# Performance work log

Hardware: AMD Instinct MI355X
Metric: run time of the kernel (lower is better)

Reference implementation:

```python
import jax, jax.numpy as jnp
import numpy as np

SHAPES = [(64, 64), (32, 32), (16, 16), (8, 8)]  # (H,W) per level, strides 8..64 of a 512px image
D, NH, NLV, NP, NLAYERS, DFF = 256, 8, 4, 4, 6, 1024
HD = D // NH
B = 4


def setup_inputs() -> dict:
    key = jax.random.key(0)
    ks = jax.random.split(key, 32)
    inp = {}
    for l, (h, w) in enumerate(SHAPES):
        inp[f"src{l}"] = jax.random.normal(ks[l], (B, D, h, w), jnp.float32)
        inp[f"pos{l}"] = jax.random.normal(ks[4 + l], (B, D, h, w), jnp.float32)
    s = 0.02
    p = lambda k, shape: jax.random.normal(k, shape, jnp.float32) * s
    inp["level_embed"] = p(ks[8], (NLV, D))
    inp["W_so"] = p(ks[9], (NLAYERS, D, NH * NLV * NP * 2)); inp["b_so"] = p(ks[10], (NLAYERS, NH * NLV * NP * 2))
    inp["W_aw"] = p(ks[11], (NLAYERS, D, NH * NLV * NP)); inp["b_aw"] = p(ks[12], (NLAYERS, NH * NLV * NP))
    inp["W_v"] = p(ks[13], (NLAYERS, D, D)); inp["b_v"] = p(ks[14], (NLAYERS, D))
    inp["W_o"] = p(ks[15], (NLAYERS, D, D)); inp["b_o"] = p(ks[16], (NLAYERS, D))
    inp["g1"] = jnp.ones((NLAYERS, D)); inp["be1"] = jnp.zeros((NLAYERS, D))
    inp["W_f1"] = p(ks[17], (NLAYERS, D, DFF)); inp["b_f1"] = p(ks[18], (NLAYERS, DFF))
    inp["W_f2"] = p(ks[19], (NLAYERS, DFF, D)); inp["b_f2"] = p(ks[20], (NLAYERS, D))
    inp["g2"] = jnp.ones((NLAYERS, D)); inp["be2"] = jnp.zeros((NLAYERS, D))
    return inp


def _layernorm(x, g, b):
    m = x.mean(-1, keepdims=True)
    v = x.var(-1, keepdims=True)
    return (x - m) * jax.lax.rsqrt(v + 1e-5) * g + b


def _reference_points():
    refs = []
    for (H_, W_) in SHAPES:
        ry = (jnp.arange(H_, dtype=jnp.float32) + 0.5) / H_
        rx = (jnp.arange(W_, dtype=jnp.float32) + 0.5) / W_
        gy, gx = jnp.meshgrid(ry, rx, indexing="ij")
        refs.append(jnp.stack([gx.ravel(), gy.ravel()], -1))
    return jnp.concatenate(refs, 0)  # [S,2] (x,y); valid_ratios==1 so same per level


def _ms_deform_sample(value, loc, aw):
    # value [B,S,NH,HD]; loc [B,S,NH,NLV,NP,2] (x,y in [0,1]); aw [B,S,NH,NLV,NP]
    Bq, S = value.shape[:2]
    v = value.transpose(0, 2, 1, 3)  # [B,NH,S,HD]
    out = jnp.zeros((Bq, NH, S, HD), value.dtype)
    start = 0
    for l, (H_, W_) in enumerate(SHAPES):
        n = H_ * W_
        vl = v[:, :, start:start + n, :]  # [B,NH,H_*W_,HD]
        start += n
        # grid_sample(align_corners=False) semantics: pixel = loc*size - 0.5, zero padding
        x = loc[:, :, :, l, :, 0] * W_ - 0.5  # [B,S,NH,NP]
        y = loc[:, :, :, l, :, 1] * H_ - 0.5
        x0 = jnp.floor(x); y0 = jnp.floor(y)
        wx1 = x - x0; wy1 = y - y0
        acc = jnp.zeros((Bq, NH, S * NP, HD), value.dtype)
        corners = ((0, 0, (1 - wx1) * (1 - wy1)), (1, 0, wx1 * (1 - wy1)),
                   (0, 1, (1 - wx1) * wy1), (1, 1, wx1 * wy1))
        for dx, dy, wgt in corners:
            xi = x0 + dx; yi = y0 + dy
            valid = (xi >= 0) & (xi < W_) & (yi >= 0) & (yi < H_)
            idx = (jnp.clip(yi, 0, H_ - 1) * W_ + jnp.clip(xi, 0, W_ - 1)).astype(jnp.int32)
            idx = idx.transpose(0, 2, 1, 3).reshape(Bq, NH, S * NP)
            w = (wgt * valid).transpose(0, 2, 1, 3).reshape(Bq, NH, S * NP)
            g = jnp.take_along_axis(vl, idx[..., None], axis=2)  # [B,NH,S*NP,HD]
            acc = acc + w[..., None] * g
        acc = acc.reshape(Bq, NH, S, NP, HD)
        awl = aw[:, :, :, l, :].transpose(0, 2, 1, 3)  # [B,NH,S,NP]
        out = out + (acc * awl[..., None]).sum(3)
    return out.transpose(0, 2, 1, 3).reshape(Bq, S, D)


def reference(src0, src1, src2, src3, pos0, pos1, pos2, pos3, level_embed,
              W_so, b_so, W_aw, b_aw, W_v, b_v, W_o, b_o, g1, be1,
              W_f1, b_f1, W_f2, b_f2, g2, be2):
    srcs = [src0, src1, src2, src3]
    poss = [pos0, pos1, pos2, pos3]
    src_flat, pos_flat = [], []
    for l in range(NLV):
        src_flat.append(srcs[l].reshape(B, D, -1).transpose(0, 2, 1))
        pos_flat.append(poss[l].reshape(B, D, -1).transpose(0, 2, 1) + level_embed[l])
    src = jnp.concatenate(src_flat, 1)   # [B,S,D]
    pos = jnp.concatenate(pos_flat, 1)
    S = src.shape[1]
    ref = _reference_points()  # [S,2]
    normalizer = jnp.array([[w, h] for (h, w) in SHAPES], jnp.float32)  # [NLV,2] = (W,H)

    out = src
    for i in range(NLAYERS):
        q = out + pos
        off = (q @ W_so[i] + b_so[i]).reshape(B, S, NH, NLV, NP, 2)
        loc = ref[None, :, None, None, None, :] + off / normalizer[None, None, None, :, None, :]
        aw = jax.nn.softmax((q @ W_aw[i] + b_aw[i]).reshape(B, S, NH, NLV * NP), -1)
        aw = aw.reshape(B, S, NH, NLV, NP)
        val = (out @ W_v[i] + b_v[i]).reshape(B, S, NH, HD)
        att = _ms_deform_sample(val, loc, aw) @ W_o[i] + b_o[i]
        x = _layernorm(out + att, g1[i], be1[i])
        ffn = jax.nn.relu(x @ W_f1[i] + b_f1[i]) @ W_f2[i] + b_f2[i]
        out = _layernorm(x + ffn, g2[i], be2[i])

    spatial_shapes = jnp.array(SHAPES, jnp.int32)
    level_start_index = jnp.concatenate([jnp.zeros((1,), jnp.int32),
                                         jnp.cumsum(spatial_shapes.prod(1))[:-1]])
    return out, spatial_shapes, level_start_index
```

## Files before the change

kernel.cpp:

```cpp
#include <hip/hip_runtime.h>
#include <cstdint>

#define SSn 5440
#define TTn 21760
#define TD ((size_t)TTn*256)
#define NL 6

typedef short bf16x8 __attribute__((ext_vector_type(8)));
typedef float f32x4 __attribute__((ext_vector_type(4)));
typedef float f32x2 __attribute__((ext_vector_type(2)));
typedef unsigned short u16x4 __attribute__((ext_vector_type(4)));
typedef unsigned short ushort_t;

__device__ __forceinline__ ushort_t f2b(float f) {
  uint32_t x = __float_as_uint(f);
  uint32_t r = x + 0x7FFFu + ((x >> 16) & 1u);
  return (ushort_t)(r >> 16);
}
__device__ __forceinline__ float b2f(ushort_t u) {
  return __uint_as_float((uint32_t)u << 16);
}

__global__ __launch_bounds__(256) void prep_kernel(
    const float* __restrict__ s0, const float* __restrict__ p0,
    const float* __restrict__ s1, const float* __restrict__ p1,
    const float* __restrict__ s2, const float* __restrict__ p2,
    const float* __restrict__ s3, const float* __restrict__ p3,
    const float* __restrict__ lev,
    float* __restrict__ cur, ushort_t* __restrict__ cur_b,
    ushort_t* __restrict__ pos_b, ushort_t* __restrict__ q_b)
{
  __shared__ float ts[64][65];
  __shared__ float tp[64][65];
  int bx = blockIdx.x;
  int b = bx / 340, r = bx % 340;
  const float *sp, *pp; int l, HW, start, dt, ptile;
  if (r < 256)      { l=0; HW=4096; start=0;    sp=s0; pp=p0; dt=r>>6;       ptile=r&63; }
  else if (r < 320) { l=1; HW=1024; start=4096; sp=s1; pp=p1; dt=(r-256)>>4; ptile=(r-256)&15; }
  else if (r < 336) { l=2; HW=256;  start=5120; sp=s2; pp=p2; dt=(r-320)>>2; ptile=(r-320)&3; }
  else              { l=3; HW=64;   start=5376; sp=s3; pp=p3; dt=r-336;      ptile=0; }
  int d0 = dt * 64, pp0 = ptile * 64;
  int t = threadIdx.x;
  int rr = t >> 2, c4 = (t & 3) * 16;
  size_t ibase = ((size_t)b * 256 + d0 + rr) * HW + pp0;
  #pragma unroll
  for (int i = 0; i < 4; ++i) {
    f32x4 v = *(const f32x4*)(sp + ibase + c4 + i * 4);
    f32x4 w = *(const f32x4*)(pp + ibase + c4 + i * 4);
    #pragma unroll
    for (int j = 0; j < 4; ++j) { ts[c4 + i*4 + j][rr] = v[j]; tp[c4 + i*4 + j][rr] = w[j]; }
  }
  __syncthreads();
  int token = start + pp0 + rr;
  size_t obase = ((size_t)b * SSn + token) * 256 + d0;
  #pragma unroll
  for (int i = 0; i < 4; ++i) {
    f32x4 cv; u16x4 cb, pb, qb;
    #pragma unroll
    for (int j = 0; j < 4; ++j) {
      float c = ts[rr][c4 + i*4 + j];
      float p = tp[rr][c4 + i*4 + j] + lev[l * 256 + d0 + c4 + i*4 + j];
      cv[j] = c; cb[j] = f2b(c); pb[j] = f2b(p); qb[j] = f2b(c + p);
    }
    *(f32x4*)(cur + obase + c4 + i*4) = cv;
    *(u16x4*)(cur_b + obase + c4 + i*4) = cb;
    *(u16x4*)(pos_b + obase + c4 + i*4) = pb;
    *(u16x4*)(q_b + obase + c4 + i*4) = qb;
  }
}

__global__ __launch_bounds__(256) void wprep_kernel(
    const float* __restrict__ W_so, const float* __restrict__ W_aw,
    const float* __restrict__ W_v,  const float* __restrict__ W_o,
    const float* __restrict__ W_f1, const float* __restrict__ W_f2,
    ushort_t* __restrict__ wt)
{
  __shared__ float tile[64][65];
  int bx = blockIdx.x;
  int layer = bx / 184, r = bx % 184;
  int type, ti;
  if (r < 16)       { type = 0; ti = r; }
  else if (r < 24)  { type = 1; ti = r - 16; }
  else if (r < 40)  { type = 2; ti = r - 24; }
  else if (r < 56)  { type = 3; ti = r - 40; }
  else if (r < 120) { type = 4; ti = r - 56; }
  else              { type = 5; ti = r - 120; }
  const float* src;
  int K, N, dof;
  switch (type) {
    case 0: src = W_so + (size_t)layer * 65536;  K = 256;  N = 256;  dof = 0;      break;
    case 1: src = W_aw + (size_t)layer * 32768;  K = 256;  N = 128;  dof = 65536;  break;
    case 2: src = W_v  + (size_t)layer * 65536;  K = 256;  N = 256;  dof = 98304;  break;
    case 3: src = W_o  + (size_t)layer * 65536;  K = 256;  N = 256;  dof = 163840; break;
    case 4: src = W_f1 + (size_t)layer * 262144; K = 256;  N = 1024; dof = 229376; break;
    default:src = W_f2 + (size_t)layer * 262144; K = 1024; N = 256;  dof = 491520; break;
  }
  int Kt = K >> 6;
  int k0 = (ti % Kt) * 64, n0 = (ti / Kt) * 64;
  ushort_t* dst = wt + (size_t)layer * 753664 + dof;
  int t = threadIdx.x;
  int rr = t >> 2, c4 = (t & 3) * 16;
  #pragma unroll
  for (int i = 0; i < 4; ++i) {
    f32x4 v = *(const f32x4*)(src + (size_t)(k0 + rr) * N + n0 + c4 + i * 4);
    tile[c4 + i*4 + 0][rr] = v[0];
    tile[c4 + i*4 + 1][rr] = v[1];
    tile[c4 + i*4 + 2][rr] = v[2];
    tile[c4 + i*4 + 3][rr] = v[3];
  }
  __syncthreads();
  #pragma unroll
  for (int i = 0; i < 4; ++i) {
    u16x4 o;
    #pragma unroll
    for (int j = 0; j < 4; ++j) o[j] = f2b(tile[rr][c4 + i*4 + j]);
    *(u16x4*)(dst + (size_t)(n0 + rr) * K + k0 + c4 + i * 4) = o;
  }
}

__global__ void bias_fuse(const float* __restrict__ bso,
                          const float* __restrict__ baw,
                          float* __restrict__ bsa)
{
  int l = blockIdx.x, t = threadIdx.x;
  bsa[l * 384 + t] = (t < 256) ? bso[l * 256 + t] : baw[l * 128 + t - 256];
}

__device__ __forceinline__ void gemm_body(
    ushort_t* As, ushort_t* Bs,
    const ushort_t* __restrict__ A, const ushort_t* __restrict__ Bt,
    const float* __restrict__ bias, ushort_t* __restrict__ Cb,
    int N, int n0, int m0, int K, int relu)
{
  int t = threadIdx.x;
  int l = t & 63, w = t >> 6;
  int wr = w >> 1, wc = w & 1;
  int lq = l >> 4, l15 = l & 15, r7 = l & 7;
  f32x4 acc[4][4] = {};

  for (int k0 = 0; k0 < K; k0 += 64) {
    #pragma unroll
    for (int i = 0; i < 4; ++i) {
      int c = i * 256 + t;
      int row = c >> 3;
      int sc = (c & 7) ^ (row & 7);
      __builtin_amdgcn_global_load_lds(
          (const uint32_t*)(A + (size_t)(m0 + row) * K + k0 + sc * 8),
          (uint32_t*)((char*)As + c * 16), 16, 0, 0);
      __builtin_amdgcn_global_load_lds(
          (const uint32_t*)(Bt + (size_t)(n0 + row) * K + k0 + sc * 8),
          (uint32_t*)((char*)Bs + c * 16), 16, 0, 0);
    }
    __syncthreads();
    #pragma unroll
    for (int ks = 0; ks < 2; ++ks) {
      bf16x8 af[4], bfr[4];
      int chs = ((ks << 2) + lq) ^ r7;
      #pragma unroll
      for (int mt = 0; mt < 4; ++mt)
        af[mt] = *(const bf16x8*)((const char*)As +
                   (wr * 64 + mt * 16 + l15) * 128 + (chs << 4));
      #pragma unroll
      for (int nt = 0; nt < 4; ++nt)
        bfr[nt] = *(const bf16x8*)((const char*)Bs +
                   (wc * 64 + nt * 16 + l15) * 128 + (chs << 4));
      #pragma unroll
      for (int mt = 0; mt < 4; ++mt)
        #pragma unroll
        for (int nt = 0; nt < 4; ++nt)
          acc[mt][nt] = __builtin_amdgcn_mfma_f32_16x16x32_bf16(
              af[mt], bfr[nt], acc[mt][nt], 0, 0, 0);
    }
    __syncthreads();
  }

  int crow0 = m0 + wr * 64;
  int ccol0 = n0 + wc * 64;
  #pragma unroll
  for (int mt = 0; mt < 4; ++mt) {
    #pragma unroll
    for (int nt = 0; nt < 4; ++nt) {
      int col = ccol0 + nt * 16 + l15;
      float bv = bias[col];
      #pragma unroll
      for (int r = 0; r < 4; ++r) {
        int rowg = crow0 + mt * 16 + lq * 4 + r;
        float v = acc[mt][nt][r] + bv;
        if (relu) v = fmaxf(v, 0.f);
        Cb[(size_t)rowg * N + col] = f2b(v);
      }
    }
  }
}

__global__ __launch_bounds__(256) void gemm_mfma(
    const ushort_t* __restrict__ A, const ushort_t* __restrict__ Bt,
    const float* __restrict__ bias, ushort_t* __restrict__ Cb,
    int N, int K, int relu)
{
  __shared__ alignas(16) ushort_t As[8192];
  __shared__ alignas(16) ushort_t Bs[8192];
  gemm_body(As, Bs, A, Bt, bias, Cb, N, blockIdx.y * 128, blockIdx.x * 128, K, relu);
}

__global__ __launch_bounds__(256) void gemm_dual(
    const ushort_t* __restrict__ A0, const ushort_t* __restrict__ Bt0,
    const float* __restrict__ bias0, ushort_t* __restrict__ C0,
    const ushort_t* __restrict__ A1, const ushort_t* __restrict__ Bt1,
    const float* __restrict__ bias1, ushort_t* __restrict__ C1,
    int K)
{
  __shared__ alignas(16) ushort_t As[8192];
  __shared__ alignas(16) ushort_t Bs[8192];
  int gy = blockIdx.y;
  if (gy < 3)
    gemm_body(As, Bs, A0, Bt0, bias0, C0, 384, gy * 128, blockIdx.x * 128, K, 0);
  else
    gemm_body(As, Bs, A1, Bt1, bias1, C1, 256, (gy - 3) * 128, blockIdx.x * 128, K, 0);
}

__global__ __launch_bounds__(256) void gemm_ln(
    const ushort_t* __restrict__ A, const ushort_t* __restrict__ Bt,
    const float* __restrict__ bias, const float* __restrict__ res,
    const float* __restrict__ g, const float* __restrict__ be,
    float* __restrict__ Of, ushort_t* __restrict__ Ob,
    ushort_t* __restrict__ Oq, const ushort_t* __restrict__ posb,
    int K)
{
  __shared__ alignas(16) ushort_t As[32 * 64];
  __shared__ alignas(16) ushort_t Bs[256 * 64];
  __shared__ float psum[32][4];
  __shared__ float psum2[32][4];
  __shared__ float2 mstd[32];
  int t = threadIdx.x;
  int l = t & 63, w = t >> 6;
  int m0 = blockIdx.x * 32;
  int lq = l >> 4, l15 = l & 15, r7 = l & 7;
  f32x4 acc[2][4] = {};

  for (int k0 = 0; k0 < K; k0 += 64) {
    {
      int c = t;
      int row = c >> 3;
      int sc = (c & 7) ^ (row & 7);
      __builtin_amdgcn_global_load_lds(
          (const uint32_t*)(A + (size_t)(m0 + row) * K + k0 + sc * 8),
          (uint32_t*)((char*)As + c * 16), 16, 0, 0);
    }
    #pragma unroll
    for (int i = 0; i < 8; ++i) {
      int c = i * 256 + t;
      int row = c >> 3;
      int sc = (c & 7) ^ (row & 7);
      __builtin_amdgcn_global_load_lds(
          (const uint32_t*)(Bt + (size_t)row * K + k0 + sc * 8),
          (uint32_t*)((char*)Bs + c * 16), 16, 0, 0);
    }
    __syncthreads();
    #pragma unroll
    for (int ks = 0; ks < 2; ++ks) {
      bf16x8 af[2], bfr[4];
      int chs = ((ks << 2) + lq) ^ r7;
      #pragma unroll
      for (int mt = 0; mt < 2; ++mt)
        af[mt] = *(const bf16x8*)((const char*)As +
                   (mt * 16 + l15) * 128 + (chs << 4));
      #pragma unroll
      for (int nt = 0; nt < 4; ++nt)
        bfr[nt] = *(const bf16x8*)((const char*)Bs +
                   (w * 64 + nt * 16 + l15) * 128 + (chs << 4));
      #pragma unroll
      for (int mt = 0; mt < 2; ++mt)
        #pragma unroll
        for (int nt = 0; nt < 4; ++nt)
          acc[mt][nt] = __builtin_amdgcn_mfma_f32_16x16x32_bf16(
              af[mt], bfr[nt], acc[mt][nt], 0, 0, 0);
    }
    __syncthreads();
  }

  float gv[4], bev[4], biasv[4];
  #pragma unroll
  for (int nt = 0; nt < 4; ++nt) {
    int col = w * 64 + nt * 16 + l15;
    gv[nt] = g[col]; bev[nt] = be[col]; biasv[nt] = bias[col];
  }
  #pragma unroll
  for (int mt = 0; mt < 2; ++mt) {
    #pragma unroll
    for (int r = 0; r < 4; ++r) {
      int rowg = m0 + mt * 16 + lq * 4 + r;
      #pragma unroll
      for (int nt = 0; nt < 4; ++nt) {
        int col = w * 64 + nt * 16 + l15;
        acc[mt][nt][r] += biasv[nt] + res[(size_t)rowg * 256 + col];
      }
    }
  }
  #pragma unroll
  for (int mt = 0; mt < 2; ++mt) {
    #pragma unroll
    for (int r = 0; r < 4; ++r) {
      float s = 0.f, s2 = 0.f;
      #pragma unroll
      for (int nt = 0; nt < 4; ++nt) {
        float v = acc[mt][nt][r];
        s += v; s2 += v * v;
      }
      #pragma unroll
      for (int off = 1; off < 16; off <<= 1) {
        s  += __shfl_xor(s, off);
        s2 += __shfl_xor(s2, off);
      }
      if (l15 == 0) {
        int rloc = mt * 16 + lq * 4 + r;
        psum[rloc][w] = s;
        psum2[rloc][w] = s2;
      }
    }
  }
  __syncthreads();
  if (t < 32) {
    f32x4 a = *(const f32x4*)psum[t];
    f32x4 b = *(const f32x4*)psum2[t];
    float s = a[0] + a[1] + a[2] + a[3];
    float s2 = b[0] + b[1] + b[2] + b[3];
    float mean = s * (1.f / 256.f);
    float var = s2 * (1.f / 256.f) - mean * mean;
    mstd[t] = make_float2(mean, rsqrtf(var + 1e-5f));
  }
  __syncthreads();
  #pragma unroll
  for (int mt = 0; mt < 2; ++mt) {
    #pragma unroll
    for (int r = 0; r < 4; ++r) {
      int rloc = mt * 16 + lq * 4 + r;
      int rowg = m0 + rloc;
      float2 ms = mstd[rloc];
      #pragma unroll
      for (int nt = 0; nt < 4; ++nt) {
        int col = w * 64 + nt * 16 + l15;
        float y = (acc[mt][nt][r] - ms.x) * ms.y * gv[nt] + bev[nt];
        size_t o = (size_t)rowg * 256 + col;
        Of[o] = y;
        Ob[o] = f2b(y);
        if (Oq) Oq[o] = f2b(y + b2f(posb[o]));
      }
    }
  }
}

__global__ __launch_bounds__(256, 8) void sample_kernel(
    const ushort_t* __restrict__ val, const ushort_t* __restrict__ sa,
    ushort_t* __restrict__ att)
{
  __shared__ uint4 rec[8][136];
  int tid = threadIdx.x;
  int bid = blockIdx.x;
  int t0 = ((bid & 7) * 340 + (bid >> 3)) * 8;

  #pragma unroll
  for (int it = 0; it < 4; ++it) {
    int idx = it * 256 + tid;
    int tl = idx >> 7;
    int pt = idx & 127;
    int t = t0 + tl;
    int b = t / SSn, s = t % SSn;
    int lvl = (pt >> 2) & 3;
    int st, Wt;
    if (s < 4096)      { st = 0;    Wt = 64; }
    else if (s < 5120) { st = 4096; Wt = 32; }
    else if (s < 5376) { st = 5120; Wt = 16; }
    else               { st = 5376; Wt = 8;  }
    int p = s - st;
    int iy = p / Wt, ix = p % Wt;
    float refx = (ix + 0.5f) / Wt;
    float refy = (iy + 0.5f) / Wt;

    float logit = b2f(sa[(size_t)t * 384 + 256 + pt]);
    float m = logit;
    #pragma unroll
    for (int off = 1; off < 16; off <<= 1) m = fmaxf(m, __shfl_xor(m, off));
    float e = __expf(logit - m);
    float sum = e;
    #pragma unroll
    for (int off = 1; off < 16; off <<= 1) sum += __shfl_xor(sum, off);
    float wa = e / sum;

    const int LWt[4] = {64, 32, 16, 8};
    const int LST[4] = {0, 4096, 5120, 5376};
    int Wl = LWt[lvl], Hl = Wl, stl = LST[lvl];

    float ox = b2f(sa[(size_t)t * 384 + pt * 2]);
    float oy = b2f(sa[(size_t)t * 384 + pt * 2 + 1]);
    float x = refx * Wl + ox - 0.5f;
    float y = refy * Hl + oy - 0.5f;
    float x0f = floorf(x), y0f = floorf(y);
    int x0 = (int)x0f, y0 = (int)y0f;
    float wx1 = x - x0f, wy1 = y - y0f;
    int vbase = b * SSn + stl;
    uint32_t ipk[4]; uint32_t wpk[4];
    #pragma unroll
    for (int c = 0; c < 4; ++c) {
      int dx = c & 1, dy = c >> 1;
      int xi = x0 + dx, yi = y0 + dy;
      float wgt = (dx ? wx1 : 1.f - wx1) * (dy ? wy1 : 1.f - wy1);
      bool valid = (xi >= 0) & (xi < Wl) & (yi >= 0) & (yi < Hl);
      int xc = min(max(xi, 0), Wl - 1), yc = min(max(yi, 0), Hl - 1);
      ipk[c] = (uint32_t)(vbase + yc * Wl + xc);
      wpk[c] = valid ? (uint32_t)f2b(wgt * wa) : 0u;
    }
    uint4 r;
    r.x = ipk[0] | (ipk[1] << 16);
    r.y = ipk[2] | (ipk[3] << 16);
    r.z = wpk[0] | (wpk[1] << 16);
    r.w = wpk[2] | (wpk[3] << 16);
    rec[tl][pt + (pt >> 4)] = r;
  }
  __syncthreads();

  int tl = tid >> 5, v = tid & 31;
  int t = t0 + tl;
  int h = v >> 2, j = v & 3;
  int c0 = h * 32 + j * 8;
  f32x2 ac[4] = {};
  #pragma unroll
  for (int k = 0; k < 16; ++k) {
    uint4 r = rec[tl][h * 17 + k];
    uint32_t id[4] = { r.x & 0xFFFFu, r.x >> 16, r.y & 0xFFFFu, r.y >> 16 };
    float wv[4] = { __uint_as_float(r.z << 16),
                    __uint_as_float(r.z & 0xFFFF0000u),
                    __uint_as_float(r.w << 16),
                    __uint_as_float(r.w & 0xFFFF0000u) };
    #pragma unroll
    for (int c = 0; c < 4; ++c) {
      uint4 uv = *(const uint4*)(val + ((size_t)id[c] << 8) + c0);
      f32x2 w2 = {wv[c], wv[c]};
      f32x2 p0 = {__uint_as_float(uv.x << 16), __uint_as_float(uv.x & 0xFFFF0000u)};
      f32x2 p1 = {__uint_as_float(uv.y << 16), __uint_as_float(uv.y & 0xFFFF0000u)};
      f32x2 p2 = {__uint_as_float(uv.z << 16), __uint_as_float(uv.z & 0xFFFF0000u)};
      f32x2 p3 = {__uint_as_float(uv.w << 16), __uint_as_float(uv.w & 0xFFFF0000u)};
      ac[0] += w2 * p0;
      ac[1] += w2 * p1;
      ac[2] += w2 * p2;
      ac[3] += w2 * p3;
    }
  }
  uint4 pk;
  pk.x = (uint32_t)f2b(ac[0][0]) | ((uint32_t)f2b(ac[0][1]) << 16);
  pk.y = (uint32_t)f2b(ac[1][0]) | ((uint32_t)f2b(ac[1][1]) << 16);
  pk.z = (uint32_t)f2b(ac[2][0]) | ((uint32_t)f2b(ac[2][1]) << 16);
  pk.w = (uint32_t)f2b(ac[3][0]) | ((uint32_t)f2b(ac[3][1]) << 16);
  *(uint4*)(att + (size_t)t * 256 + c0) = pk;
}

__global__ void tail_kernel(float* __restrict__ o) {
  const float v[12] = {64.f, 64.f, 32.f, 32.f, 16.f, 16.f, 8.f, 8.f,
                       0.f, 4096.f, 5120.f, 5376.f};
  int i = threadIdx.x;
  if (i < 12) o[i] = v[i];
}

extern "C" void kernel_launch(void* const* d_in, const int* in_sizes, int n_in,
                              void* d_out, int out_size, void* d_ws, size_t ws_size,
                              hipStream_t stream)
{
  const float* s0  = (const float*)d_in[0];
  const float* p0  = (const float*)d_in[1];
  const float* s1  = (const float*)d_in[2];
  const float* p1  = (const float*)d_in[3];
  const float* s2  = (const float*)d_in[4];
  const float* p2  = (const float*)d_in[5];
  const float* s3  = (const float*)d_in[6];
  const float* p3  = (const float*)d_in[7];
  const float* lev = (const float*)d_in[8];
  const float* W_so = (const float*)d_in[9];
  const float* b_so = (const float*)d_in[10];
  const float* W_aw = (const float*)d_in[11];
  const float* b_aw = (const float*)d_in[12];
  const float* W_v  = (const float*)d_in[13];
  const float* b_v  = (const float*)d_in[14];
  const float* W_o  = (const float*)d_in[15];
  const float* b_o  = (const float*)d_in[16];
  const float* g1   = (const float*)d_in[17];
  const float* be1  = (const float*)d_in[18];
  const float* W_f1 = (const float*)d_in[19];
  const float* b_f1 = (const float*)d_in[20];
  const float* W_f2 = (const float*)d_in[21];
  const float* b_f2 = (const float*)d_in[22];
  const float* g2   = (const float*)d_in[23];
  const float* be2  = (const float*)d_in[24];

  float* out = (float*)d_out;
  float* ws  = (float*)d_ws;

  ushort_t* pos_b = (ushort_t*)ws;
  float*    x_f   = ws + TD / 2;
  ushort_t* q_b   = (ushort_t*)(ws + TD / 2 + TD);
  ushort_t* cur_b = (ushort_t*)(ws + 2 * TD);
  ushort_t* x_b   = (ushort_t*)(ws + 2 * TD + TD / 2);
  ushort_t* sa_b  = (ushort_t*)(ws + 3 * TD);
  ushort_t* val_b = (ushort_t*)(ws + 3 * TD + 3 * (TD / 4));
  ushort_t* h_b   = (ushort_t*)(ws + 3 * TD);
  ushort_t* wt    = (ushort_t*)(ws + 5 * TD);
  float*    bsa   = ws + 5 * TD + 2260992;

  const size_t LW = 753664;

  wprep_kernel<<<1104, 256, 0, stream>>>(W_so, W_aw, W_v, W_o, W_f1, W_f2, wt);
  bias_fuse<<<NL, 384, 0, stream>>>(b_so, b_aw, bsa);
  prep_kernel<<<1360, 256, 0, stream>>>(s0, p0, s1, p1, s2, p2, s3, p3, lev,
                                        out, cur_b, pos_b, q_b);

  for (int i = 0; i < NL; ++i) {
    ushort_t* wl = wt + (size_t)i * LW;
    const float* bv  = b_v  + (size_t)i * 256;
    const float* bo  = b_o  + (size_t)i * 256;
    const float* bf1 = b_f1 + (size_t)i * 1024;
    const float* bf2 = b_f2 + (size_t)i * 256;

    gemm_dual<<<dim3(170, 5), 256, 0, stream>>>(q_b, wl + 0, bsa + i * 384, sa_b,
                                                cur_b, wl + 98304, bv, val_b, 256);
    sample_kernel<<<TTn / 8, 256, 0, stream>>>(val_b, sa_b, q_b);
    gemm_ln<<<680, 256, 0, stream>>>(q_b, wl + 163840, bo, out,
                                     g1 + i * 256, be1 + i * 256,
                                     x_f, x_b, nullptr, nullptr, 256);
    gemm_mfma<<<dim3(170, 8), 256, 0, stream>>>(x_b, wl + 229376, bf1,
                                                h_b, 1024, 256, 1);
    gemm_ln<<<680, 256, 0, stream>>>(h_b, wl + 491520, bf2, x_f,
                                     g2 + i * 256, be2 + i * 256,
                                     out, cur_b, q_b, pos_b, 1024);
  }

  tail_kernel<<<1, 16, 0, stream>>>(out + TD);
}
```

Before: 790.0 us.

## Permute weight output columns so GEMM epilogues store contiguous 4-wide vectors

```diff
diff --git a/kernel.cpp b/kernel.cpp
--- a/kernel.cpp
+++ b/kernel.cpp
@@ -109,12 +109,13 @@
     tile[c4 + i*4 + 3][rr] = v[3];
   }
   __syncthreads();
+  int vrow = ((rr & 3) << 4) | (rr >> 2);
   #pragma unroll
   for (int i = 0; i < 4; ++i) {
     u16x4 o;
     #pragma unroll
     for (int j = 0; j < 4; ++j) o[j] = f2b(tile[rr][c4 + i*4 + j]);
-    *(u16x4*)(dst + (size_t)(n0 + rr) * K + k0 + c4 + i * 4) = o;
+    *(u16x4*)(dst + (size_t)(n0 + vrow) * K + k0 + c4 + i * 4) = o;
   }
 }
 
@@ -175,20 +176,21 @@
   }
 
   int crow0 = m0 + wr * 64;
-  int ccol0 = n0 + wc * 64;
+  int cb = n0 + wc * 64 + l15 * 4;
+  f32x4 bv4 = *(const f32x4*)(bias + cb);
   #pragma unroll
   for (int mt = 0; mt < 4; ++mt) {
     #pragma unroll
-    for (int nt = 0; nt < 4; ++nt) {
-      int col = ccol0 + nt * 16 + l15;
-      float bv = bias[col];
-      #pragma unroll
-      for (int r = 0; r < 4; ++r) {
-        int rowg = crow0 + mt * 16 + lq * 4 + r;
-        float v = acc[mt][nt][r] + bv;
+    for (int r = 0; r < 4; ++r) {
+      int rowg = crow0 + mt * 16 + lq * 4 + r;
+      u16x4 o;
+      #pragma unroll
+      for (int nt = 0; nt < 4; ++nt) {
+        float v = acc[mt][nt][r] + bv4[nt];
         if (relu) v = fmaxf(v, 0.f);
-        Cb[(size_t)rowg * N + col] = f2b(v);
+        o[nt] = f2b(v);
       }
+      *(u16x4*)(Cb + (size_t)rowg * N + cb) = o;
     }
   }
 }
@@ -279,22 +281,19 @@
     __syncthreads();
   }
 
-  float gv[4], bev[4], biasv[4];
-  #pragma unroll
-  for (int nt = 0; nt < 4; ++nt) {
-    int col = w * 64 + nt * 16 + l15;
-    gv[nt] = g[col]; bev[nt] = be[col]; biasv[nt] = bias[col];
-  }
+  int cb = w * 64 + l15 * 4;
+  f32x4 g4 = *(const f32x4*)(g + cb);
+  f32x4 be4 = *(const f32x4*)(be + cb);
+  f32x4 b4 = *(const f32x4*)(bias + cb);
   #pragma unroll
   for (int mt = 0; mt < 2; ++mt) {
     #pragma unroll
     for (int r = 0; r < 4; ++r) {
       int rowg = m0 + mt * 16 + lq * 4 + r;
-      #pragma unroll
-      for (int nt = 0; nt < 4; ++nt) {
-        int col = w * 64 + nt * 16 + l15;
-        acc[mt][nt][r] += biasv[nt] + res[(size_t)rowg * 256 + col];
-      }
+      f32x4 r4 = *(const f32x4*)(res + (size_t)rowg * 256 + cb);
+      #pragma unroll
+      for (int nt = 0; nt < 4; ++nt)
+        acc[mt][nt][r] += b4[nt] + r4[nt];
     }
   }
   #pragma unroll
@@ -337,20 +336,27 @@
       int rloc = mt * 16 + lq * 4 + r;
       int rowg = m0 + rloc;
       float2 ms = mstd[rloc];
+      size_t o = (size_t)rowg * 256 + cb;
+      f32x4 y4; u16x4 yb;
       #pragma unroll
       for (int nt = 0; nt < 4; ++nt) {
-        int col = w * 64 + nt * 16 + l15;
-        float y = (acc[mt][nt][r] - ms.x) * ms.y * gv[nt] + bev[nt];
-        size_t o = (size_t)rowg * 256 + col;
-        Of[o] = y;
-        Ob[o] = f2b(y);
-        if (Oq) Oq[o] = f2b(y + b2f(posb[o]));
+        float y = (acc[mt][nt][r] - ms.x) * ms.y * g4[nt] + be4[nt];
+        y4[nt] = y; yb[nt] = f2b(y);
       }
-    }
-  }
-}
-
-__global__ __launch_bounds__(256, 8) void sample_kernel(
+      *(f32x4*)(Of + o) = y4;
+      *(u16x4*)(Ob + o) = yb;
+      if (Oq) {
+        u16x4 p4 = *(const u16x4*)(posb + o);
+        u16x4 q4;
+        #pragma unroll
+        for (int nt = 0; nt < 4; ++nt) q4[nt] = f2b(y4[nt] + b2f(p4[nt]));
+        *(u16x4*)(Oq + o) = q4;
+      }
+    }
+  }
+}
+
+__global__ __launch_bounds__(256, 6) void sample_kernel(
     const ushort_t* __restrict__ val, const ushort_t* __restrict__ sa,
     ushort_t* __restrict__ att)
 {
```

New measurement: 753.4 us. 1.05x faster.
